# Performance work log

Measured on AMD Instinct MI355X. Metric: run time of the kernel, lower is better.

The kernel has to match this reference:

```python
import jax, jax.numpy as jnp
import numpy as np

ATOM_FDIM = 133
BOND_FDIM = 147
HIDDEN = 300
DEPTH = 3
N_ATOMS = 100000
N_BONDS = 200000
MAX_NB = 6
N_MOLS = 4000


def setup_inputs() -> dict:
    key = jax.random.key(0)
    ks = jax.random.split(key, 10)
    f_atoms = jax.random.normal(ks[0], (N_ATOMS, ATOM_FDIM), dtype=jnp.float32)
    f_bonds = jax.random.normal(ks[1], (N_BONDS, BOND_FDIM), dtype=jnp.float32)
    a2b = jax.random.randint(ks[2], (N_ATOMS, MAX_NB), 0, N_BONDS)
    b2a = jax.random.randint(ks[3], (N_BONDS,), 0, N_ATOMS)
    b2revb = jax.random.randint(ks[4], (N_BONDS,), 0, N_BONDS)
    atom2mol = jnp.sort(jax.random.randint(ks[5], (N_ATOMS,), 0, N_MOLS))
    s = 1.0 / np.sqrt(HIDDEN)
    W_i = jax.random.uniform(ks[6], (BOND_FDIM, HIDDEN), jnp.float32, -s, s)
    W_h = jax.random.uniform(ks[7], (HIDDEN, HIDDEN), jnp.float32, -s, s)
    W_o_w = jax.random.uniform(ks[8], (ATOM_FDIM + HIDDEN, HIDDEN), jnp.float32, -s, s)
    W_o_b = jax.random.uniform(ks[9], (HIDDEN,), jnp.float32, -s, s)
    return {"f_atoms": f_atoms, "f_bonds": f_bonds, "a2b": a2b, "b2a": b2a,
            "b2revb": b2revb, "atom2mol": atom2mol, "W_i": W_i, "W_h": W_h,
            "W_o_w": W_o_w, "W_o_b": W_o_b}


def reference(f_atoms, f_bonds, a2b, b2a, b2revb, atom2mol, W_i, W_h, W_o_w, W_o_b):
    # input = W_i(f_bonds); message = act(input)
    inp = f_bonds @ W_i                      # [n_bonds, hidden]
    message = jax.nn.relu(inp)
    for _ in range(DEPTH - 1):
        # gather neighbor bond messages per atom and sum: [n_atoms, max_nb, h] -> [n_atoms, h]
        a_message = message[a2b].sum(axis=1)
        rev_message = message[b2revb]        # [n_bonds, hidden]
        message = a_message[b2a] - rev_message
        message = jax.nn.relu(inp + message @ W_h)
    # final atom-level aggregation
    a_message = message[a2b].sum(axis=1)     # [n_atoms, hidden]
    a_input = jnp.concatenate([f_atoms, a_message], axis=1)
    atom_hiddens = jax.nn.relu(a_input @ W_o_w + W_o_b)
    # segment mean pooling over molecules
    sums = jax.ops.segment_sum(atom_hiddens, atom2mol, num_segments=N_MOLS)
    counts = jax.ops.segment_sum(jnp.ones((atom_hiddens.shape[0],), atom_hiddens.dtype),
                                 atom2mol, num_segments=N_MOLS)
    mol_vecs = sums / jnp.maximum(counts, 1.0)[:, None]  # zero vec for empty mols
    return mol_vecs
```

## Files before the change

### kernel.cpp

```cpp
#include <hip/hip_runtime.h>
#include <stdint.h>

#define ATOM_FDIM 133
#define BOND_FDIM 147
#define HIDDEN    300
#define N_ATOMS   100000
#define N_BONDS   200000
#define MAX_NB    6
#define N_MOLS    4000

#define KP_I 160
#define KP_H 320
#define KP_O 448
#define LDA  304
#define CPR  38

#define TM   128
#define ACH  8
#define BCH  24

typedef unsigned short u16;
typedef short bf16x8 __attribute__((ext_vector_type(8)));
typedef float f32x4 __attribute__((ext_vector_type(4)));

__device__ __forceinline__ u16 f2bu(float f) {
    unsigned u = __float_as_uint(f);
    u += 0x7FFFu + ((u >> 16) & 1u);
    return (u16)(u >> 16);
}
__device__ __forceinline__ float bu2f(u16 b) { return __uint_as_float(((unsigned)b) << 16); }

#define AS1 __attribute__((address_space(1)))
#define AS3 __attribute__((address_space(3)))
__device__ __forceinline__ void gl_lds16(const void* g, void* l) {
    __builtin_amdgcn_global_load_lds((const AS1 void*)g, (AS3 void*)l, 16, 0, 0);
}

template <int EPI>
__global__ __launch_bounds__(512, 2) void mm_k(
    const u16* __restrict__ A, int lda,
    const u16* __restrict__ Wp,
    const float* __restrict__ bias,
    u16* __restrict__ out0, int ldo0,
    u16* __restrict__ out1, int ldo1,
    int M, int NT)
{
    __shared__ __align__(16) u16 As[4 * ACH * 512];
    __shared__ __align__(16) u16 Bs[4 * BCH * 512];

    const int t    = threadIdx.x;
    const int lane = t & 63, wid = t >> 6;
    const int fl   = lane & 15, fh = lane >> 4;
    const int m0   = blockIdx.x * TM;
    const int wr   = wid >> 1, wc = wid & 1;

    int arow = m0 + wid * 16 + fl;
    if (arow > M - 1) arow = M - 1;
    const size_t srcA = (size_t)arow * (size_t)lda * 2u + (size_t)(fh * 16);
    const size_t srcB = (size_t)(3 * wid) * 1024u + (size_t)lane * 16u;

    char* ldsAbase = (char*)As + wid * 1024;
    char* ldsBbase = (char*)Bs + 3 * wid * 1024;

#define STAGE(buf, kt) do {                                               \
        const size_t kbA_ = (size_t)(kt) * 64u;                           \
        const size_t kbB_ = (size_t)(kt) * (size_t)(BCH * 1024);          \
        char* la_ = ldsAbase + (size_t)(buf) * (ACH * 1024);              \
        char* lb_ = ldsBbase + (size_t)(buf) * (BCH * 1024);              \
        gl_lds16((const char*)A + srcA + kbA_, la_);                      \
        gl_lds16((const char*)Wp + kbB_ + srcB,        lb_);              \
        gl_lds16((const char*)Wp + kbB_ + srcB + 1024, lb_ + 1024);       \
        gl_lds16((const char*)Wp + kbB_ + srcB + 2048, lb_ + 2048);       \
    } while (0)

    f32x4 acc[2][12] = {};

    STAGE(0, 0);
    STAGE(1, 1);
    STAGE(2, 2);
    asm volatile("s_waitcnt vmcnt(8)" ::: "memory");
    __builtin_amdgcn_s_barrier();

    int cur = 0;
    for (int tt = 0; tt < NT; ++tt) {
        int w3 = tt + 3; if (w3 >= NT) w3 -= NT;
        const int nx3 = (cur + 3) & 3;
        STAGE(nx3, w3);

        const u16* as_c = As + cur * (ACH * 512);
        const u16* bs_c = Bs + cur * (BCH * 512);
        bf16x8 af0, af1, bfv[12];
        af0 = *reinterpret_cast<const bf16x8*>(&as_c[(wr * 2 + 0) * 512 + lane * 8]);
        af1 = *reinterpret_cast<const bf16x8*>(&as_c[(wr * 2 + 1) * 512 + lane * 8]);
        #pragma unroll
        for (int n = 0; n < 12; ++n)
            bfv[n] = *reinterpret_cast<const bf16x8*>(&bs_c[(wc * 12 + n) * 512 + lane * 8]);

        __builtin_amdgcn_s_setprio(1);
        #pragma unroll
        for (int n = 0; n < 12; ++n) {
            acc[0][n] = __builtin_amdgcn_mfma_f32_16x16x32_bf16(af0, bfv[n], acc[0][n], 0, 0, 0);
            acc[1][n] = __builtin_amdgcn_mfma_f32_16x16x32_bf16(af1, bfv[n], acc[1][n], 0, 0, 0);
        }
        __builtin_amdgcn_s_setprio(0);

        asm volatile("s_waitcnt vmcnt(8)" ::: "memory");
        __builtin_amdgcn_s_barrier();

        cur = (cur + 1) & 3;
    }
#undef STAGE

    #pragma unroll
    for (int m = 0; m < 2; ++m) {
        #pragma unroll
        for (int r = 0; r < 4; ++r) {
            const int row = m0 + wr * 32 + m * 16 + fh * 4 + r;
            if (row >= M) continue;
            #pragma unroll
            for (int n = 0; n < 12; ++n) {
                const int col = wc * 192 + n * 16 + fl;
                if (col >= HIDDEN) continue;
                const float v = acc[m][n][r];
                if (EPI == 0) {
                    out0[(size_t)row * ldo0 + col] = f2bu(v);
                    out1[(size_t)row * ldo1 + col] = f2bu(fmaxf(v, 0.f));
                } else if (EPI == 1) {
                    out0[(size_t)row * ldo0 + col] = f2bu(v);
                } else {
                    out0[(size_t)row * ldo0 + col] = f2bu(fmaxf(v + bias[col], 0.f));
                }
            }
        }
    }
}

__global__ __launch_bounds__(256) void wconv_k(const float* __restrict__ W,
                                               int split, int off1, int Ktot, int NT,
                                               u16* __restrict__ Wp)
{
    const int id = blockIdx.x * 256 + threadIdx.x;
    if (id >= NT * BCH * 512) return;
    const int block = id >> 9, rem = id & 511;
    const int l = rem >> 3, e = rem & 7;
    const int c = block % BCH, kt = block / BCH;
    const int col = c * 16 + (l & 15);
    const int k   = kt * 32 + (l >> 4) * 8 + e;
    float v = 0.f;
    if (col < HIDDEN) {
        if (k < split) {
            const int r = k + off1;
            if (r < Ktot) v = W[(size_t)r * HIDDEN + col];
        } else {
            const int r = k - split;
            if (r < off1) v = W[(size_t)r * HIDDEN + col];
        }
    }
    Wp[id] = f2bu(v);
}

__global__ __launch_bounds__(256) void fbconv_k(const float* __restrict__ fb, u16* __restrict__ dst)
{
    const int id = blockIdx.x * 256 + threadIdx.x;
    if (id >= N_BONDS * KP_I) return;
    const int r = id / KP_I, k = id - r * KP_I;
    dst[id] = f2bu(k < BOND_FDIM ? fb[(size_t)r * BOND_FDIM + k] : 0.f);
}

__global__ __launch_bounds__(256) void agg_k(const u16* __restrict__ src,
                                             const int* __restrict__ a2b,
                                             u16* __restrict__ dst)
{
    const int c = blockIdx.x * 256 + threadIdx.x;
    if (c >= N_ATOMS * CPR) return;
    const int a = c / CPR, q = c - a * CPR;
    const int h = q * 8;
    const int* nb = a2b + (size_t)a * MAX_NB;
    float s[8] = {};
    #pragma unroll
    for (int j = 0; j < MAX_NB; ++j) {
        const int r = nb[j];
        union { uint4 u; u16 s[8]; } x;
        x.u = *(const uint4*)(src + (size_t)r * LDA + h);
        #pragma unroll
        for (int e = 0; e < 8; ++e) s[e] += bu2f(x.s[e]);
    }
    union { uint4 u; u16 s[8]; } o;
    #pragma unroll
    for (int e = 0; e < 8; ++e) o.s[e] = f2bu(s[e]);
    *(uint4*)(dst + (size_t)a * LDA + h) = o.u;
}

__global__ __launch_bounds__(256) void comb_k(const u16* __restrict__ inp,
                                              const u16* __restrict__ aY,
                                              const u16* __restrict__ Y,
                                              const int* __restrict__ b2a,
                                              const int* __restrict__ b2revb,
                                              u16* __restrict__ msg)
{
    const int c = blockIdx.x * 256 + threadIdx.x;
    if (c >= N_BONDS * CPR) return;
    const int b = c / CPR, q = c - b * CPR;
    const int h = q * 8;
    const int ia = b2a[b], ir = b2revb[b];
    union { uint4 u; u16 s[8]; } xi, xa, xy, o;
    xi.u = *(const uint4*)(inp + (size_t)b * LDA + h);
    xa.u = *(const uint4*)(aY + (size_t)ia * LDA + h);
    xy.u = *(const uint4*)(Y + (size_t)ir * LDA + h);
    #pragma unroll
    for (int j = 0; j < 8; ++j)
        o.s[j] = f2bu(fmaxf(bu2f(xi.s[j]) + bu2f(xa.s[j]) - bu2f(xy.s[j]), 0.f));
    *(uint4*)(msg + (size_t)b * LDA + h) = o.u;
}

__global__ __launch_bounds__(256) void aggcat_k(const u16* __restrict__ msg,
                                                const int* __restrict__ a2b,
                                                const float* __restrict__ fa,
                                                u16* __restrict__ dst)
{
    const int id = blockIdx.x * 256 + threadIdx.x;
    if (id >= N_ATOMS * (KP_O / 4)) return;
    const int a = id / (KP_O / 4), c = id - a * (KP_O / 4);
    const int e0 = c * 4;
    union { uint2 u; u16 s[4]; } o;
    if (e0 < HIDDEN) {
        const int* nb = a2b + (size_t)a * MAX_NB;
        float s0 = 0.f, s1 = 0.f, s2 = 0.f, s3 = 0.f;
        #pragma unroll
        for (int j = 0; j < MAX_NB; ++j) {
            union { uint2 u; u16 s[4]; } x;
            x.u = *(const uint2*)(msg + (size_t)nb[j] * LDA + e0);
            s0 += bu2f(x.s[0]); s1 += bu2f(x.s[1]); s2 += bu2f(x.s[2]); s3 += bu2f(x.s[3]);
        }
        o.s[0] = f2bu(s0); o.s[1] = f2bu(s1); o.s[2] = f2bu(s2); o.s[3] = f2bu(s3);
    } else {
        #pragma unroll
        for (int j = 0; j < 4; ++j) {
            const int fi = e0 + j - HIDDEN;
            o.s[j] = (fi < ATOM_FDIM) ? f2bu(fa[(size_t)a * ATOM_FDIM + fi]) : (u16)0;
        }
    }
    *(uint2*)(dst + (size_t)a * KP_O + e0) = o.u;
}

__global__ __launch_bounds__(320) void pool_k(const u16* __restrict__ ah,
                                              const int* __restrict__ a2m,
                                              float* __restrict__ out)
{
    const int m = blockIdx.x;
    int lo, hi;
    { int l = 0, r = N_ATOMS;
      while (l < r) { int mid = (l + r) >> 1; if (a2m[mid] < m) l = mid + 1; else r = mid; }
      lo = l; }
    { int l = lo, r = N_ATOMS;
      while (l < r) { int mid = (l + r) >> 1; if (a2m[mid] < m + 1) l = mid + 1; else r = mid; }
      hi = l; }
    const float inv = 1.0f / (float)((hi - lo) > 1 ? (hi - lo) : 1);
    const int h = threadIdx.x;
    if (h >= HIDDEN) return;
    float s = 0.f;
    for (int a = lo; a < hi; ++a) s += bu2f(ah[(size_t)a * LDA + h]);
    out[(size_t)m * HIDDEN + h] = s * inv;
}

extern "C" void kernel_launch(void* const* d_in, const int* in_sizes, int n_in,
                              void* d_out, int out_size, void* d_ws, size_t ws_size,
                              hipStream_t stream)
{
    const float* f_atoms  = (const float*)d_in[0];
    const float* f_bonds  = (const float*)d_in[1];
    const int*   a2b      = (const int*)d_in[2];
    const int*   b2a      = (const int*)d_in[3];
    const int*   b2revb   = (const int*)d_in[4];
    const int*   atom2mol = (const int*)d_in[5];
    const float* W_i      = (const float*)d_in[6];
    const float* W_h      = (const float*)d_in[7];
    const float* W_o_w    = (const float*)d_in[8];
    const float* W_o_b    = (const float*)d_in[9];
    float* out = (float*)d_out;

    char* p = (char*)d_ws;
    auto alloc = [&](size_t bytes) { char* r = p; p += (bytes + 255) & ~(size_t)255; return r; };
    u16* inp = (u16*)alloc(((size_t)N_BONDS + 16) * LDA * 2);
    u16* msg = (u16*)alloc(((size_t)N_BONDS + 16) * LDA * 2);
    u16* Yb  = (u16*)alloc(((size_t)N_BONDS + 16) * LDA * 2);
    u16* aY  = (u16*)alloc(((size_t)N_ATOMS + 16) * LDA * 2);
    u16* Wpi = (u16*)alloc((size_t)(KP_I / 32) * BCH * 512 * 2);
    u16* Wph = (u16*)alloc((size_t)(KP_H / 32) * BCH * 512 * 2);
    u16* Wpo = (u16*)alloc((size_t)(KP_O / 32) * BCH * 512 * 2);
    if ((size_t)(p - (char*)d_ws) > ws_size) return;

    u16* fb16   = Yb;
    u16* concat = Yb;
    u16* ah     = msg;

    const dim3 blk(256);
    auto g1 = [](long long n) { return dim3((unsigned)((n + 255) / 256)); };
    const dim3 blk5(512);
    const dim3 gB((N_BONDS + TM - 1) / TM);
    const dim3 gA((N_ATOMS + TM - 1) / TM);

    const int BIGSPLIT = 1 << 20;
    wconv_k<<<g1((long long)(KP_I / 32) * BCH * 512), blk, 0, stream>>>(
        W_i, BIGSPLIT, 0, BOND_FDIM, KP_I / 32, Wpi);
    wconv_k<<<g1((long long)(KP_H / 32) * BCH * 512), blk, 0, stream>>>(
        W_h, BIGSPLIT, 0, HIDDEN, KP_H / 32, Wph);
    wconv_k<<<g1((long long)(KP_O / 32) * BCH * 512), blk, 0, stream>>>(
        W_o_w, HIDDEN, ATOM_FDIM, ATOM_FDIM + HIDDEN, KP_O / 32, Wpo);
    fbconv_k<<<g1((long long)N_BONDS * KP_I), blk, 0, stream>>>(f_bonds, fb16);

    mm_k<0><<<gB, blk5, 0, stream>>>(fb16, KP_I, Wpi, nullptr,
                                     inp, LDA, msg, LDA, N_BONDS, KP_I / 32);

    for (int it = 0; it < 2; ++it) {
        mm_k<1><<<gB, blk5, 0, stream>>>(msg, LDA, Wph, nullptr,
                                         Yb, LDA, nullptr, 0, N_BONDS, KP_H / 32);
        agg_k<<<g1((long long)N_ATOMS * CPR), blk, 0, stream>>>(Yb, a2b, aY);
        comb_k<<<g1((long long)N_BONDS * CPR), blk, 0, stream>>>(inp, aY, Yb, b2a, b2revb, msg);
    }

    aggcat_k<<<g1((long long)N_ATOMS * (KP_O / 4)), blk, 0, stream>>>(msg, a2b, f_atoms, concat);
    mm_k<2><<<gA, blk5, 0, stream>>>(concat, KP_O, Wpo, W_o_b,
                                     ah, LDA, nullptr, 0, N_ATOMS, KP_O / 32);
    pool_k<<<dim3(N_MOLS), dim3(320), 0, stream>>>(ah, atom2mol, out);
}
```

Baseline: 950.7 us.

## Fuse relu and message-combine prologues into GEMM A-tile loading

The first GEMM now writes only the pre-activation input, and the next GEMM applies ReLU while staging its A tile through registers into LDS. The second message-passing GEMM gathers aY[b2a] and Y[b2revb] per row and computes relu(inp + aY - Y) on the fly, which removes one comb_k launch and its full message write/read. The main loop also changes from a 4-stage to a 3-stage LDS pipeline with the B loads split into half-steps and extra barriers. In exchange, the A operand now goes through register loads, ALU conversion and LDS stores instead of direct global-to-LDS copies, and there is more synchronisation per k-step.

New measurement: 884.4 us. 7.0% less time.

```diff
diff --git a/kernel.cpp b/kernel.cpp
--- a/kernel.cpp
+++ b/kernel.cpp
@@ -30,23 +30,42 @@
 }
 __device__ __forceinline__ float bu2f(u16 b) { return __uint_as_float(((unsigned)b) << 16); }
 
+__device__ __forceinline__ uint4 relu_bf16x8(uint4 v) {
+    union { uint4 u; u16 s[8]; } x, o;
+    x.u = v;
+    #pragma unroll
+    for (int e = 0; e < 8; ++e) o.s[e] = (x.s[e] & 0x8000u) ? (u16)0 : x.s[e];
+    return o.u;
+}
+__device__ __forceinline__ uint4 comb_bf16x8(uint4 vi, uint4 va, uint4 vy) {
+    union { uint4 u; u16 s[8]; } xi, xa, xy, o;
+    xi.u = vi; xa.u = va; xy.u = vy;
+    #pragma unroll
+    for (int e = 0; e < 8; ++e)
+        o.s[e] = f2bu(fmaxf(bu2f(xi.s[e]) + bu2f(xa.s[e]) - bu2f(xy.s[e]), 0.f));
+    return o.u;
+}
+
 #define AS1 __attribute__((address_space(1)))
 #define AS3 __attribute__((address_space(3)))
-__device__ __forceinline__ void gl_lds16(const void* g, void* l) {
+__device__ __forceinline__ void gl_lds(const void* g, void* l) {
     __builtin_amdgcn_global_load_lds((const AS1 void*)g, (AS3 void*)l, 16, 0, 0);
 }
 
-template <int EPI>
+template <int AM, int EPI>
 __global__ __launch_bounds__(512, 2) void mm_k(
     const u16* __restrict__ A, int lda,
+    const u16* __restrict__ aYp,
+    const u16* __restrict__ Yp,
+    const int* __restrict__ b2a,
+    const int* __restrict__ b2revb,
     const u16* __restrict__ Wp,
     const float* __restrict__ bias,
     u16* __restrict__ out0, int ldo0,
-    u16* __restrict__ out1, int ldo1,
     int M, int NT)
 {
-    __shared__ __align__(16) u16 As[4 * ACH * 512];
-    __shared__ __align__(16) u16 Bs[4 * BCH * 512];
+    __shared__ __align__(16) u16 As[3][ACH * 512];
+    __shared__ __align__(16) u16 Bs[3][BCH * 512];
 
     const int t    = threadIdx.x;
     const int lane = t & 63, wid = t >> 6;
@@ -56,60 +75,121 @@
 
     int arow = m0 + wid * 16 + fl;
     if (arow > M - 1) arow = M - 1;
-    const size_t srcA = (size_t)arow * (size_t)lda * 2u + (size_t)(fh * 16);
+    const char* srcAp = (const char*)A + (size_t)arow * (size_t)lda * 2u + (size_t)(fh * 16);
+    const char* pI = srcAp;
+    const char* pA = nullptr; const char* pY = nullptr;
+    if constexpr (AM == 2) {
+        const int ia = b2a[arow], ir = b2revb[arow];
+        pA = (const char*)aYp + (size_t)ia * (LDA * 2) + (size_t)(fh * 16);
+        pY = (const char*)Yp  + (size_t)ir * (LDA * 2) + (size_t)(fh * 16);
+    }
+    const char* WpC = (const char*)Wp;
     const size_t srcB = (size_t)(3 * wid) * 1024u + (size_t)lane * 16u;
 
-    char* ldsAbase = (char*)As + wid * 1024;
-    char* ldsBbase = (char*)Bs + 3 * wid * 1024;
-
-#define STAGE(buf, kt) do {                                               \
-        const size_t kbA_ = (size_t)(kt) * 64u;                           \
-        const size_t kbB_ = (size_t)(kt) * (size_t)(BCH * 1024);          \
-        char* la_ = ldsAbase + (size_t)(buf) * (ACH * 1024);              \
-        char* lb_ = ldsBbase + (size_t)(buf) * (BCH * 1024);              \
-        gl_lds16((const char*)A + srcA + kbA_, la_);                      \
-        gl_lds16((const char*)Wp + kbB_ + srcB,        lb_);              \
-        gl_lds16((const char*)Wp + kbB_ + srcB + 1024, lb_ + 1024);       \
-        gl_lds16((const char*)Wp + kbB_ + srcB + 2048, lb_ + 2048);       \
-    } while (0)
-
     f32x4 acc[2][12] = {};
-
-    STAGE(0, 0);
-    STAGE(1, 1);
-    STAGE(2, 2);
-    asm volatile("s_waitcnt vmcnt(8)" ::: "memory");
-    __builtin_amdgcn_s_barrier();
-
-    int cur = 0;
-    for (int tt = 0; tt < NT; ++tt) {
-        int w3 = tt + 3; if (w3 >= NT) w3 -= NT;
-        const int nx3 = (cur + 3) & 3;
-        STAGE(nx3, w3);
-
-        const u16* as_c = As + cur * (ACH * 512);
-        const u16* bs_c = Bs + cur * (BCH * 512);
-        bf16x8 af0, af1, bfv[12];
-        af0 = *reinterpret_cast<const bf16x8*>(&as_c[(wr * 2 + 0) * 512 + lane * 8]);
-        af1 = *reinterpret_cast<const bf16x8*>(&as_c[(wr * 2 + 1) * 512 + lane * 8]);
-        #pragma unroll
-        for (int n = 0; n < 12; ++n)
-            bfv[n] = *reinterpret_cast<const bf16x8*>(&bs_c[(wc * 12 + n) * 512 + lane * 8]);
-
-        __builtin_amdgcn_s_setprio(1);
-        #pragma unroll
-        for (int n = 0; n < 12; ++n) {
-            acc[0][n] = __builtin_amdgcn_mfma_f32_16x16x32_bf16(af0, bfv[n], acc[0][n], 0, 0, 0);
-            acc[1][n] = __builtin_amdgcn_mfma_f32_16x16x32_bf16(af1, bfv[n], acc[1][n], 0, 0, 0);
-        }
-        __builtin_amdgcn_s_setprio(0);
-
-        asm volatile("s_waitcnt vmcnt(8)" ::: "memory");
+    uint4 qa0, qa1, qa2, qb0, qb1, qb2;
+    (void)qa1; (void)qa2; (void)qb1; (void)qb2;
+
+    if constexpr (AM == 0) {
+        gl_lds(srcAp, (char*)As[0] + wid * 1024);
+        #pragma unroll
+        for (int j = 0; j < 3; ++j) gl_lds(WpC + srcB + (size_t)j * 1024, (char*)Bs[0] + 3 * wid * 1024 + j * 1024);
+        gl_lds(srcAp + 64, (char*)As[1] + wid * 1024);
+        #pragma unroll
+        for (int j = 0; j < 3; ++j) gl_lds(WpC + (size_t)(BCH * 1024) + srcB + (size_t)j * 1024, (char*)Bs[1] + 3 * wid * 1024 + j * 1024);
+        asm volatile("s_waitcnt vmcnt(4)" ::: "memory");
         __builtin_amdgcn_s_barrier();
-
-        cur = (cur + 1) & 3;
-    }
-#undef STAGE
+    } else if constexpr (AM == 1) {
+        qb0 = *reinterpret_cast<const uint4*>(pI);
+        #pragma unroll
+        for (int j = 0; j < 3; ++j) gl_lds(WpC + srcB + (size_t)j * 1024, (char*)Bs[0] + 3 * wid * 1024 + j * 1024);
+        qa0 = *reinterpret_cast<const uint4*>(pI + 64);
+        #pragma unroll
+        for (int j = 0; j < 3; ++j) gl_lds(WpC + (size_t)(BCH * 1024) + srcB + (size_t)j * 1024, (char*)Bs[1] + 3 * wid * 1024 + j * 1024);
+        asm volatile("s_waitcnt vmcnt(4)" ::: "memory");
+        *reinterpret_cast<uint4*>(&As[0][wid * 512 + lane * 8]) = relu_bf16x8(qb0);
+        asm volatile("s_waitcnt lgkmcnt(0)" ::: "memory");
+        __builtin_amdgcn_s_barrier();
+    } else {
+        qb0 = *reinterpret_cast<const uint4*>(pI);
+        qb1 = *reinterpret_cast<const uint4*>(pA);
+        qb2 = *reinterpret_cast<const uint4*>(pY);
+        #pragma unroll
+        for (int j = 0; j < 3; ++j) gl_lds(WpC + srcB + (size_t)j * 1024, (char*)Bs[0] + 3 * wid * 1024 + j * 1024);
+        qa0 = *reinterpret_cast<const uint4*>(pI + 64);
+        qa1 = *reinterpret_cast<const uint4*>(pA + 64);
+        qa2 = *reinterpret_cast<const uint4*>(pY + 64);
+        #pragma unroll
+        for (int j = 0; j < 3; ++j) gl_lds(WpC + (size_t)(BCH * 1024) + srcB + (size_t)j * 1024, (char*)Bs[1] + 3 * wid * 1024 + j * 1024);
+        asm volatile("s_waitcnt vmcnt(6)" ::: "memory");
+        *reinterpret_cast<uint4*>(&As[0][wid * 512 + lane * 8]) = comb_bf16x8(qb0, qb1, qb2);
+        asm volatile("s_waitcnt lgkmcnt(0)" ::: "memory");
+        __builtin_amdgcn_s_barrier();
+    }
+
+    int tt = 0, cur = 0;
+
+#define STEP(RNi, RNa, RNy, RXi, RXa, RXy) do {                                             \
+    int w2 = tt + 2; if (w2 >= NT) w2 -= NT;                                                \
+    const int nx1 = (cur < 2) ? cur + 1 : 0;                                                \
+    const int nx2 = (nx1 < 2) ? nx1 + 1 : 0;                                                \
+    bf16x8 af0, af1, bfv[12];                                                               \
+    af0 = *reinterpret_cast<const bf16x8*>(&As[cur][(wr * 2 + 0) * 512 + lane * 8]);        \
+    af1 = *reinterpret_cast<const bf16x8*>(&As[cur][(wr * 2 + 1) * 512 + lane * 8]);        \
+    _Pragma("unroll")                                                                       \
+    for (int n = 0; n < 6; ++n)                                                             \
+        bfv[n] = *reinterpret_cast<const bf16x8*>(&Bs[cur][(wc * 12 + n) * 512 + lane * 8]);\
+    if constexpr (AM == 0) {                                                                \
+        gl_lds(srcAp + (size_t)w2 * 64u, (char*)As[nx2] + wid * 1024);                      \
+    } else if constexpr (AM == 1) {                                                         \
+        RXi = *reinterpret_cast<const uint4*>(pI + (size_t)w2 * 64u);                       \
+    } else {                                                                                \
+        RXi = *reinterpret_cast<const uint4*>(pI + (size_t)w2 * 64u);                       \
+        RXa = *reinterpret_cast<const uint4*>(pA + (size_t)w2 * 64u);                       \
+        RXy = *reinterpret_cast<const uint4*>(pY + (size_t)w2 * 64u);                       \
+    }                                                                                       \
+    gl_lds(WpC + (size_t)w2 * (size_t)(BCH * 1024) + srcB, (char*)Bs[nx2] + 3 * wid * 1024);\
+    __builtin_amdgcn_s_barrier();                                                           \
+    __builtin_amdgcn_s_setprio(1);                                                          \
+    _Pragma("unroll")                                                                       \
+    for (int n = 0; n < 6; ++n) {                                                           \
+        acc[0][n] = __builtin_amdgcn_mfma_f32_16x16x32_bf16(af0, bfv[n], acc[0][n], 0,0,0); \
+        acc[1][n] = __builtin_amdgcn_mfma_f32_16x16x32_bf16(af1, bfv[n], acc[1][n], 0,0,0); \
+    }                                                                                       \
+    __builtin_amdgcn_s_setprio(0);                                                          \
+    __builtin_amdgcn_s_barrier();                                                           \
+    _Pragma("unroll")                                                                       \
+    for (int n = 6; n < 12; ++n)                                                            \
+        bfv[n] = *reinterpret_cast<const bf16x8*>(&Bs[cur][(wc * 12 + n) * 512 + lane * 8]);\
+    gl_lds(WpC + (size_t)w2 * (size_t)(BCH * 1024) + srcB + 1024, (char*)Bs[nx2] + 3 * wid * 1024 + 1024); \
+    gl_lds(WpC + (size_t)w2 * (size_t)(BCH * 1024) + srcB + 2048, (char*)Bs[nx2] + 3 * wid * 1024 + 2048); \
+    if constexpr (AM == 2) { asm volatile("s_waitcnt vmcnt(6)" ::: "memory"); }             \
+    else                   { asm volatile("s_waitcnt vmcnt(4)" ::: "memory"); }             \
+    if constexpr (AM == 1) {                                                                \
+        *reinterpret_cast<uint4*>(&As[nx1][wid * 512 + lane * 8]) = relu_bf16x8(RNi);       \
+        asm volatile("s_waitcnt lgkmcnt(0)" ::: "memory");                                  \
+    } else if constexpr (AM == 2) {                                                         \
+        *reinterpret_cast<uint4*>(&As[nx1][wid * 512 + lane * 8]) = comb_bf16x8(RNi, RNa, RNy); \
+        asm volatile("s_waitcnt lgkmcnt(0)" ::: "memory");                                  \
+    }                                                                                       \
+    __builtin_amdgcn_s_barrier();                                                           \
+    __builtin_amdgcn_s_setprio(1);                                                          \
+    _Pragma("unroll")                                                                       \
+    for (int n = 6; n < 12; ++n) {                                                          \
+        acc[0][n] = __builtin_amdgcn_mfma_f32_16x16x32_bf16(af0, bfv[n], acc[0][n], 0,0,0); \
+        acc[1][n] = __builtin_amdgcn_mfma_f32_16x16x32_bf16(af1, bfv[n], acc[1][n], 0,0,0); \
+    }                                                                                       \
+    __builtin_amdgcn_s_setprio(0);                                                          \
+    __builtin_amdgcn_s_barrier();                                                           \
+    cur = nx1; ++tt;                                                                        \
+} while (0)
+
+    while (tt + 1 < NT) {
+        STEP(qa0, qa1, qa2, qb0, qb1, qb2);
+        STEP(qb0, qb1, qb2, qa0, qa1, qa2);
+    }
+    if (tt < NT) STEP(qa0, qa1, qa2, qb0, qb1, qb2);
+#undef STEP
 
     #pragma unroll
     for (int m = 0; m < 2; ++m) {
@@ -122,14 +202,8 @@
                 const int col = wc * 192 + n * 16 + fl;
                 if (col >= HIDDEN) continue;
                 const float v = acc[m][n][r];
-                if (EPI == 0) {
-                    out0[(size_t)row * ldo0 + col] = f2bu(v);
-                    out1[(size_t)row * ldo1 + col] = f2bu(fmaxf(v, 0.f));
-                } else if (EPI == 1) {
-                    out0[(size_t)row * ldo0 + col] = f2bu(v);
-                } else {
-                    out0[(size_t)row * ldo0 + col] = f2bu(fmaxf(v + bias[col], 0.f));
-                }
+                if (EPI == 0) out0[(size_t)row * ldo0 + col] = f2bu(v);
+                else          out0[(size_t)row * ldo0 + col] = f2bu(fmaxf(v + bias[col], 0.f));
             }
         }
     }
@@ -281,18 +355,22 @@
 
     char* p = (char*)d_ws;
     auto alloc = [&](size_t bytes) { char* r = p; p += (bytes + 255) & ~(size_t)255; return r; };
-    u16* inp = (u16*)alloc(((size_t)N_BONDS + 16) * LDA * 2);
-    u16* msg = (u16*)alloc(((size_t)N_BONDS + 16) * LDA * 2);
-    u16* Yb  = (u16*)alloc(((size_t)N_BONDS + 16) * LDA * 2);
-    u16* aY  = (u16*)alloc(((size_t)N_ATOMS + 16) * LDA * 2);
+    u16* B0 = (u16*)alloc(((size_t)N_BONDS + 16) * LDA * 2);
+    u16* B1 = (u16*)alloc(((size_t)N_BONDS + 16) * LDA * 2);
+    u16* B2 = (u16*)alloc(((size_t)N_BONDS + 16) * LDA * 2);
+    u16* aY = (u16*)alloc(((size_t)N_ATOMS + 16) * LDA * 2);
     u16* Wpi = (u16*)alloc((size_t)(KP_I / 32) * BCH * 512 * 2);
     u16* Wph = (u16*)alloc((size_t)(KP_H / 32) * BCH * 512 * 2);
     u16* Wpo = (u16*)alloc((size_t)(KP_O / 32) * BCH * 512 * 2);
     if ((size_t)(p - (char*)d_ws) > ws_size) return;
 
-    u16* fb16   = Yb;
-    u16* concat = Yb;
-    u16* ah     = msg;
+    u16* inp    = B0;
+    u16* fb16   = B1;
+    u16* Y1     = B1;
+    u16* Y2     = B2;
+    u16* msg2   = B1;
+    u16* concat = B2;
+    u16* ah     = B0;
 
     const dim3 blk(256);
     auto g1 = [](long long n) { return dim3((unsigned)((n + 255) / 256)); };
@@ -309,18 +387,21 @@
         W_o_w, HIDDEN, ATOM_FDIM, ATOM_FDIM + HIDDEN, KP_O / 32, Wpo);
     fbconv_k<<<g1((long long)N_BONDS * KP_I), blk, 0, stream>>>(f_bonds, fb16);
 
-    mm_k<0><<<gB, blk5, 0, stream>>>(fb16, KP_I, Wpi, nullptr,
-                                     inp, LDA, msg, LDA, N_BONDS, KP_I / 32);
-
-    for (int it = 0; it < 2; ++it) {
-        mm_k<1><<<gB, blk5, 0, stream>>>(msg, LDA, Wph, nullptr,
-                                         Yb, LDA, nullptr, 0, N_BONDS, KP_H / 32);
-        agg_k<<<g1((long long)N_ATOMS * CPR), blk, 0, stream>>>(Yb, a2b, aY);
-        comb_k<<<g1((long long)N_BONDS * CPR), blk, 0, stream>>>(inp, aY, Yb, b2a, b2revb, msg);
-    }
-
-    aggcat_k<<<g1((long long)N_ATOMS * (KP_O / 4)), blk, 0, stream>>>(msg, a2b, f_atoms, concat);
-    mm_k<2><<<gA, blk5, 0, stream>>>(concat, KP_O, Wpo, W_o_b,
-                                     ah, LDA, nullptr, 0, N_ATOMS, KP_O / 32);
+    mm_k<0, 0><<<gB, blk5, 0, stream>>>(fb16, KP_I, nullptr, nullptr, nullptr, nullptr,
+                                        Wpi, nullptr, inp, LDA, N_BONDS, KP_I / 32);
+
+    mm_k<1, 0><<<gB, blk5, 0, stream>>>(inp, LDA, nullptr, nullptr, nullptr, nullptr,
+                                        Wph, nullptr, Y1, LDA, N_BONDS, KP_H / 32);
+    agg_k<<<g1((long long)N_ATOMS * CPR), blk, 0, stream>>>(Y1, a2b, aY);
+
+    mm_k<2, 0><<<gB, blk5, 0, stream>>>(inp, LDA, aY, Y1, b2a, b2revb,
+                                        Wph, nullptr, Y2, LDA, N_BONDS, KP_H / 32);
+    agg_k<<<g1((long long)N_ATOMS * CPR), blk, 0, stream>>>(Y2, a2b, aY);
+
+    comb_k<<<g1((long long)N_BONDS * CPR), blk, 0, stream>>>(inp, aY, Y2, b2a, b2revb, msg2);
+    aggcat_k<<<g1((long long)N_ATOMS * (KP_O / 4)), blk, 0, stream>>>(msg2, a2b, f_atoms, concat);
+
+    mm_k<0, 1><<<gA, blk5, 0, stream>>>(concat, KP_O, nullptr, nullptr, nullptr, nullptr,
+                                        Wpo, W_o_b, ah, LDA, N_ATOMS, KP_O / 32);
     pool_k<<<dim3(N_MOLS), dim3(320), 0, stream>>>(ah, atom2mol, out);
 }
```

## Trim GEMM N-tile to 320 columns and split K-loop into two-phase triple-buffered pipeline

Applied to the files above, without the earlier changes.

The GEMM kernel's N padding drops from 384 to 320 columns (BCH 24→20), cutting MFMA work and B-tile traffic spent on padding beyond HIDDEN=300. The LDS pipeline goes from 4 stages to 3, and each K step is split into two halves. The next tile's loads are issued between the halves, with per-wave vmcnt gates because waves now issue unequal load counts. Buffer aliasing in the host code is renamed and the loop is unrolled, with no semantic change. This adds more barriers per iteration and relies on wconv_k packing consistently with the new BCH, which is not shown.

Result: faster. 872.7 us (-8.2%).

```diff
diff --git a/kernel.cpp b/kernel.cpp
--- a/kernel.cpp
+++ b/kernel.cpp
@@ -17,7 +17,7 @@
 
 #define TM   128
 #define ACH  8
-#define BCH  24
+#define BCH  20
 
 typedef unsigned short u16;
 typedef short bf16x8 __attribute__((ext_vector_type(8)));
@@ -32,7 +32,7 @@
 
 #define AS1 __attribute__((address_space(1)))
 #define AS3 __attribute__((address_space(3)))
-__device__ __forceinline__ void gl_lds16(const void* g, void* l) {
+__device__ __forceinline__ void gl_lds(const void* g, void* l) {
     __builtin_amdgcn_global_load_lds((const AS1 void*)g, (AS3 void*)l, 16, 0, 0);
 }
 
@@ -45,8 +45,8 @@
     u16* __restrict__ out1, int ldo1,
     int M, int NT)
 {
-    __shared__ __align__(16) u16 As[4 * ACH * 512];
-    __shared__ __align__(16) u16 Bs[4 * BCH * 512];
+    __shared__ __align__(16) u16 As[3][ACH * 512];
+    __shared__ __align__(16) u16 Bs[3][BCH * 512];
 
     const int t    = threadIdx.x;
     const int lane = t & 63, wid = t >> 6;
@@ -56,60 +56,79 @@
 
     int arow = m0 + wid * 16 + fl;
     if (arow > M - 1) arow = M - 1;
-    const size_t srcA = (size_t)arow * (size_t)lda * 2u + (size_t)(fh * 16);
-    const size_t srcB = (size_t)(3 * wid) * 1024u + (size_t)lane * 16u;
-
-    char* ldsAbase = (char*)As + wid * 1024;
-    char* ldsBbase = (char*)Bs + 3 * wid * 1024;
-
-#define STAGE(buf, kt) do {                                               \
-        const size_t kbA_ = (size_t)(kt) * 64u;                           \
-        const size_t kbB_ = (size_t)(kt) * (size_t)(BCH * 1024);          \
-        char* la_ = ldsAbase + (size_t)(buf) * (ACH * 1024);              \
-        char* lb_ = ldsBbase + (size_t)(buf) * (BCH * 1024);              \
-        gl_lds16((const char*)A + srcA + kbA_, la_);                      \
-        gl_lds16((const char*)Wp + kbB_ + srcB,        lb_);              \
-        gl_lds16((const char*)Wp + kbB_ + srcB + 1024, lb_ + 1024);       \
-        gl_lds16((const char*)Wp + kbB_ + srcB + 2048, lb_ + 2048);       \
+    const char* srcAp = (const char*)A + (size_t)arow * (size_t)lda * 2u + (size_t)(fh * 16);
+    const char* WpC = (const char*)Wp;
+    const int bbase = (wid < 4) ? 3 * wid : 12 + 2 * (wid - 4);
+    const size_t srcB0 = (size_t)bbase * 1024u + (size_t)lane * 16u;
+
+    f32x4 acc[2][10] = {};
+
+#define STAGE_T(kt, buf) do {                                                    \
+        const size_t kbB_ = (size_t)(kt) * (size_t)(BCH * 1024);                 \
+        gl_lds(srcAp + (size_t)(kt) * 64u, (char*)As[buf] + wid * 1024);         \
+        gl_lds(WpC + kbB_ + srcB0,        (char*)Bs[buf] + bbase * 1024);        \
+        gl_lds(WpC + kbB_ + srcB0 + 1024, (char*)Bs[buf] + bbase * 1024 + 1024); \
+        if (wid < 4)                                                             \
+            gl_lds(WpC + kbB_ + srcB0 + 2048, (char*)Bs[buf] + bbase * 1024 + 2048); \
     } while (0)
 
-    f32x4 acc[2][12] = {};
-
-    STAGE(0, 0);
-    STAGE(1, 1);
-    STAGE(2, 2);
-    asm volatile("s_waitcnt vmcnt(8)" ::: "memory");
+#define GATE() do {                                                        \
+        if (wid < 4) asm volatile("s_waitcnt vmcnt(4)" ::: "memory");      \
+        else         asm volatile("s_waitcnt vmcnt(3)" ::: "memory");      \
+    } while (0)
+
+    STAGE_T(0, 0);
+    STAGE_T(1, 1);
+    GATE();
     __builtin_amdgcn_s_barrier();
 
     int cur = 0;
     for (int tt = 0; tt < NT; ++tt) {
-        int w3 = tt + 3; if (w3 >= NT) w3 -= NT;
-        const int nx3 = (cur + 3) & 3;
-        STAGE(nx3, w3);
-
-        const u16* as_c = As + cur * (ACH * 512);
-        const u16* bs_c = Bs + cur * (BCH * 512);
-        bf16x8 af0, af1, bfv[12];
+        int w2 = tt + 2; if (w2 >= NT) w2 -= NT;
+        const int nx1 = (cur < 2) ? cur + 1 : 0;
+        const int nx2 = (nx1 < 2) ? nx1 + 1 : 0;
+        const u16* as_c = As[cur];
+        const u16* bs_c = Bs[cur];
+        const size_t kbB = (size_t)w2 * (size_t)(BCH * 1024);
+
+        bf16x8 af0, af1, bfv[10];
         af0 = *reinterpret_cast<const bf16x8*>(&as_c[(wr * 2 + 0) * 512 + lane * 8]);
         af1 = *reinterpret_cast<const bf16x8*>(&as_c[(wr * 2 + 1) * 512 + lane * 8]);
         #pragma unroll
-        for (int n = 0; n < 12; ++n)
-            bfv[n] = *reinterpret_cast<const bf16x8*>(&bs_c[(wc * 12 + n) * 512 + lane * 8]);
-
+        for (int n = 0; n < 5; ++n)
+            bfv[n] = *reinterpret_cast<const bf16x8*>(&bs_c[(wc * 10 + n) * 512 + lane * 8]);
+        gl_lds(srcAp + (size_t)w2 * 64u, (char*)As[nx2] + wid * 1024);
+        gl_lds(WpC + kbB + srcB0, (char*)Bs[nx2] + bbase * 1024);
+        __builtin_amdgcn_s_barrier();
         __builtin_amdgcn_s_setprio(1);
         #pragma unroll
-        for (int n = 0; n < 12; ++n) {
+        for (int n = 0; n < 5; ++n) {
             acc[0][n] = __builtin_amdgcn_mfma_f32_16x16x32_bf16(af0, bfv[n], acc[0][n], 0, 0, 0);
             acc[1][n] = __builtin_amdgcn_mfma_f32_16x16x32_bf16(af1, bfv[n], acc[1][n], 0, 0, 0);
         }
         __builtin_amdgcn_s_setprio(0);
-
-        asm volatile("s_waitcnt vmcnt(8)" ::: "memory");
         __builtin_amdgcn_s_barrier();
 
-        cur = (cur + 1) & 3;
-    }
-#undef STAGE
+        #pragma unroll
+        for (int n = 5; n < 10; ++n)
+            bfv[n] = *reinterpret_cast<const bf16x8*>(&bs_c[(wc * 10 + n) * 512 + lane * 8]);
+        gl_lds(WpC + kbB + srcB0 + 1024, (char*)Bs[nx2] + bbase * 1024 + 1024);
+        if (wid < 4)
+            gl_lds(WpC + kbB + srcB0 + 2048, (char*)Bs[nx2] + bbase * 1024 + 2048);
+        GATE();
+        __builtin_amdgcn_s_barrier();
+        __builtin_amdgcn_s_setprio(1);
+        #pragma unroll
+        for (int n = 5; n < 10; ++n) {
+            acc[0][n] = __builtin_amdgcn_mfma_f32_16x16x32_bf16(af0, bfv[n], acc[0][n], 0, 0, 0);
+            acc[1][n] = __builtin_amdgcn_mfma_f32_16x16x32_bf16(af1, bfv[n], acc[1][n], 0, 0, 0);
+        }
+        __builtin_amdgcn_s_setprio(0);
+        __builtin_amdgcn_s_barrier();
+        cur = nx1;
+    }
+#undef STAGE_T
+#undef GATE
 
     #pragma unroll
     for (int m = 0; m < 2; ++m) {
@@ -118,8 +137,8 @@
             const int row = m0 + wr * 32 + m * 16 + fh * 4 + r;
             if (row >= M) continue;
             #pragma unroll
-            for (int n = 0; n < 12; ++n) {
-                const int col = wc * 192 + n * 16 + fl;
+            for (int n = 0; n < 10; ++n) {
+                const int col = wc * 160 + n * 16 + fl;
                 if (col >= HIDDEN) continue;
                 const float v = acc[m][n][r];
                 if (EPI == 0) {
@@ -281,18 +300,22 @@
 
     char* p = (char*)d_ws;
     auto alloc = [&](size_t bytes) { char* r = p; p += (bytes + 255) & ~(size_t)255; return r; };
-    u16* inp = (u16*)alloc(((size_t)N_BONDS + 16) * LDA * 2);
-    u16* msg = (u16*)alloc(((size_t)N_BONDS + 16) * LDA * 2);
-    u16* Yb  = (u16*)alloc(((size_t)N_BONDS + 16) * LDA * 2);
-    u16* aY  = (u16*)alloc(((size_t)N_ATOMS + 16) * LDA * 2);
+    u16* B0 = (u16*)alloc(((size_t)N_BONDS + 16) * LDA * 2);
+    u16* B1 = (u16*)alloc(((size_t)N_BONDS + 16) * LDA * 2);
+    u16* B2 = (u16*)alloc(((size_t)N_BONDS + 16) * LDA * 2);
+    u16* aY = (u16*)alloc(((size_t)N_ATOMS + 16) * LDA * 2);
     u16* Wpi = (u16*)alloc((size_t)(KP_I / 32) * BCH * 512 * 2);
     u16* Wph = (u16*)alloc((size_t)(KP_H / 32) * BCH * 512 * 2);
     u16* Wpo = (u16*)alloc((size_t)(KP_O / 32) * BCH * 512 * 2);
     if ((size_t)(p - (char*)d_ws) > ws_size) return;
 
-    u16* fb16   = Yb;
-    u16* concat = Yb;
-    u16* ah     = msg;
+    u16* inp    = B0;
+    u16* fb16   = B1;
+    u16* Y1     = B1;
+    u16* Y2     = B1;
+    u16* concat = B1;
+    u16* msg    = B2;
+    u16* ah     = B0;
 
     const dim3 blk(256);
     auto g1 = [](long long n) { return dim3((unsigned)((n + 255) / 256)); };
@@ -312,12 +335,15 @@
     mm_k<0><<<gB, blk5, 0, stream>>>(fb16, KP_I, Wpi, nullptr,
                                      inp, LDA, msg, LDA, N_BONDS, KP_I / 32);
 
-    for (int it = 0; it < 2; ++it) {
-        mm_k<1><<<gB, blk5, 0, stream>>>(msg, LDA, Wph, nullptr,
-                                         Yb, LDA, nullptr, 0, N_BONDS, KP_H / 32);
-        agg_k<<<g1((long long)N_ATOMS * CPR), blk, 0, stream>>>(Yb, a2b, aY);
-        comb_k<<<g1((long long)N_BONDS * CPR), blk, 0, stream>>>(inp, aY, Yb, b2a, b2revb, msg);
-    }
+    mm_k<1><<<gB, blk5, 0, stream>>>(msg, LDA, Wph, nullptr,
+                                     Y1, LDA, nullptr, 0, N_BONDS, KP_H / 32);
+    agg_k<<<g1((long long)N_ATOMS * CPR), blk, 0, stream>>>(Y1, a2b, aY);
+    comb_k<<<g1((long long)N_BONDS * CPR), blk, 0, stream>>>(inp, aY, Y1, b2a, b2revb, msg);
+
+    mm_k<1><<<gB, blk5, 0, stream>>>(msg, LDA, Wph, nullptr,
+                                     Y2, LDA, nullptr, 0, N_BONDS, KP_H / 32);
+    agg_k<<<g1((long long)N_ATOMS * CPR), blk, 0, stream>>>(Y2, a2b, aY);
+    comb_k<<<g1((long long)N_BONDS * CPR), blk, 0, stream>>>(inp, aY, Y2, b2a, b2revb, msg);
 
     aggcat_k<<<g1((long long)N_ATOMS * (KP_O / 4)), blk, 0, stream>>>(msg, a2b, f_atoms, concat);
     mm_k<2><<<gA, blk5, 0, stream>>>(concat, KP_O, Wpo, W_o_b,
```
